# Performance work log

Measured on AMD Instinct MI355X. Metric: run time of the kernel, lower is better.

Reference implementation:

```python
import jax, jax.numpy as jnp
import numpy as np
from jax import lax

DIM = 512
HEADS = 64
EPS_NORM = 1e-12
EPS_BN = 1e-5


def conv1x1(x, w, b):
    # x: [B,Cin,H,W], w: [Cout,Cin,1,1]
    y = lax.conv_general_dilated(x, w, (1, 1), 'SAME',
                                 dimension_numbers=('NCHW', 'OIHW', 'NCHW'))
    return y + b[None, :, None, None]


def dwconv3x3(x, w, b):
    # depthwise: w: [C,1,3,3], groups=C
    c = x.shape[1]
    y = lax.conv_general_dilated(x, w, (1, 1), 'SAME',
                                 dimension_numbers=('NCHW', 'OIHW', 'NCHW'),
                                 feature_group_count=c)
    return y + b[None, :, None, None]


def l2norm(x):
    # normalize along last axis, torch F.normalize semantics
    n = jnp.sqrt(jnp.sum(x * x, axis=-1, keepdims=True))
    return x / jnp.maximum(n, EPS_NORM)


def setup_inputs() -> dict:
    key = jax.random.key(0)
    ks = jax.random.split(key, 12)
    b, c, h, w = 2, DIM, 128, 128
    s = lambda *sh: 0.02
    inp = {
        'hsi': jax.random.normal(ks[0], (b, c, h, w), jnp.float32),
        'lidar': jax.random.normal(ks[1], (b, c, h, w), jnp.float32),
        'hsi_qkv_w': jax.random.normal(ks[2], (3 * c, c, 1, 1), jnp.float32) * 0.02,
        'hsi_qkv_b': jnp.zeros((3 * c,), jnp.float32),
        'lidar_qkv_w': jax.random.normal(ks[3], (3 * c, c, 1, 1), jnp.float32) * 0.02,
        'lidar_qkv_b': jnp.zeros((3 * c,), jnp.float32),
        'hsi_dw_w': jax.random.normal(ks[4], (3 * c, 1, 3, 3), jnp.float32) * 0.1,
        'hsi_dw_b': jnp.zeros((3 * c,), jnp.float32),
        'lidar_dw_w': jax.random.normal(ks[5], (3 * c, 1, 3, 3), jnp.float32) * 0.1,
        'lidar_dw_b': jnp.zeros((3 * c,), jnp.float32),
        'temp1': jnp.ones((HEADS, 1, 1), jnp.float32),
        'temp2': jnp.ones((HEADS, 1, 1), jnp.float32),
        'proj_w': jax.random.normal(ks[6], (c // 8, c // 4, 1, 1), jnp.float32) * 0.1,
        'proj_b': jnp.zeros((c // 8,), jnp.float32),
        'bn_gamma': jnp.ones((c // 8,), jnp.float32),
        'bn_beta': jnp.zeros((c // 8,), jnp.float32),
        'bn_mean': jnp.zeros((c // 8,), jnp.float32),
        'bn_var': jnp.ones((c // 8,), jnp.float32),
    }
    return inp


def reference(hsi, lidar, hsi_qkv_w, hsi_qkv_b, lidar_qkv_w, lidar_qkv_b,
              hsi_dw_w, hsi_dw_b, lidar_dw_w, lidar_dw_b, temp1, temp2,
              proj_w, proj_b, bn_gamma, bn_beta, bn_mean, bn_var):
    b, c, h, w = hsi.shape
    head = HEADS
    ch = c // head  # per-head channel (=8)
    hw = h * w

    def qkv(x, qkv_w, qkv_b, dw_w, dw_b):
        y = conv1x1(x, qkv_w, qkv_b)
        y = dwconv3x3(y, dw_w, dw_b)
        q, k, v = jnp.split(y, 3, axis=1)
        # b (head ch) h w -> b head ch (h w)
        r = lambda t: t.reshape(b, head, ch, hw)
        return r(q), r(k), r(v)

    hq, hk, hv = qkv(hsi, hsi_qkv_w, hsi_qkv_b, hsi_dw_w, hsi_dw_b)
    lq, lk, lv = qkv(lidar, lidar_qkv_w, lidar_qkv_b, lidar_dw_w, lidar_dw_b)

    q1, k2 = l2norm(hq), l2norm(lk)
    q2, k1 = l2norm(lq), l2norm(hk)

    # channel-attention scores: [b, head, ch, ch]
    attn1 = jnp.einsum('bhcn,bhdn->bhcd', q1, k2) * temp1[None]
    attn2 = jnp.einsum('bhcn,bhdn->bhcd', q2, k1) * temp2[None]

    # conv-based score fusion: cat -> 1x1 conv -> BN (eval) -> ReLU
    attn_cat = jnp.concatenate([attn1, attn2], axis=1)  # [b, 2*head, ch, ch]
    fused = conv1x1(attn_cat, proj_w, proj_b)           # [b, head, ch, ch]
    fused = (fused - bn_mean[None, :, None, None]) / jnp.sqrt(bn_var + EPS_BN)[None, :, None, None]
    fused = fused * bn_gamma[None, :, None, None] + bn_beta[None, :, None, None]
    fused = jax.nn.relu(fused)

    a1 = jax.nn.softmax(fused + attn1, axis=-1)
    a2 = jax.nn.softmax(fused + attn2, axis=-1)
    # dropout is identity in eval mode

    hsi_out = jnp.einsum('bhcd,bhdn->bhcn', a1, hv) + hv
    lidar_out = jnp.einsum('bhcd,bhdn->bhcn', a2, lv) + lv

    hsi_out = hsi_out.reshape(b, c, h, w) + hsi
    lidar_out = lidar_out.reshape(b, c, h, w) + lidar
    return hsi_out, lidar_out
```

## Files before the change

kernel.cpp:

```cpp
#include <hip/hip_runtime.h>
#include <hip/hip_bf16.h>

#define B2    2
#define C     512
#define HH    128
#define WW    128
#define HW    16384
#define HEADS 64

typedef __attribute__((ext_vector_type(8))) short bf16x8;
typedef __attribute__((ext_vector_type(4))) float f32x4;
typedef __attribute__((ext_vector_type(4))) unsigned u32x4;

__device__ __forceinline__ float b2f(short s) {
    union { unsigned u; float f; } x;
    x.u = ((unsigned)(unsigned short)s) << 16;
    return x.f;
}
__device__ __forceinline__ short f2b(float f) {
    unsigned u; __builtin_memcpy(&u, &f, 4);
    unsigned r = u + 0x7FFFu + ((u >> 16) & 1u);
    return (short)(r >> 16);
}
__device__ __forceinline__ unsigned cvt_pk(float lo, float hi) {
    unsigned r;
    asm("v_cvt_pk_bf16_f32 %0, %1, %2" : "=v"(r) : "v"(lo), "v"(hi));
    return r;
}

__device__ __forceinline__ void conv8(
    const short* __restrict__ plane, int row, int lane, int cg,
    const float* __restrict__ w9, float bias0, float* o)
{
    #pragma unroll
    for (int i = 0; i < 8; ++i) o[i] = bias0;
    #pragma unroll
    for (int dr = 0; dr < 3; ++dr) {
        const int r2 = row + dr - 1;
        const bool ok = (unsigned)r2 < (unsigned)HH;
        bf16x8 v = {0, 0, 0, 0, 0, 0, 0, 0};
        if (ok) v = *(const bf16x8*)(plane + (size_t)r2 * WW);
        float rv[10];
        #pragma unroll
        for (int j = 0; j < 8; ++j) rv[1 + j] = b2f(v[j]);
        const float lf = __shfl(rv[8], lane - 1);
        const float rt = __shfl(rv[1], lane + 1);
        rv[0] = (cg == 0)  ? 0.f : lf;
        rv[9] = (cg == 15) ? 0.f : rt;
        const float w0 = w9[dr * 3], w1 = w9[dr * 3 + 1], w2 = w9[dr * 3 + 2];
        #pragma unroll
        for (int i = 0; i < 8; ++i)
            o[i] += w0 * rv[i] + w1 * rv[i + 1] + w2 * rv[i + 2];
    }
}

#define BM 128
#define BN 128
#define BK 32
#define LDK 40

struct GemmJob  { const float* X; const float* W; const float* bias; short* Y; int co_off; };
struct GemmJobs { GemmJob j[8]; };

__global__ __launch_bounds__(256) void k_gemm(GemmJobs jobs)
{
    __shared__ __align__(16) short As[BM * LDK];
    __shared__ __align__(16) short Bs[BN * LDK];

    unsigned bx = blockIdx.x, by = blockIdx.y, bz = blockIdx.z;
    {
        const unsigned nx = gridDim.x, ny = gridDim.y, nz = gridDim.z;
        const unsigned nwg = nx * ny * nz;
        if ((nwg & 7u) == 0u) {
            const unsigned hw = bx + nx * (by + ny * bz);
            const unsigned lid = (hw & 7u) * (nwg >> 3) + (hw >> 3);
            bx = lid % nx;
            const unsigned rest = lid / nx;
            by = rest % ny;
            bz = rest / ny;
        }
    }

    const GemmJob jb = jobs.j[bz];
    const float* X    = jb.X;
    const float* Wm   = jb.W;
    const float* bias = jb.bias;
    short*       Y    = jb.Y;
    const int co_off  = jb.co_off;

    const int co0 = bx * BM;
    const int p0  = by * BN;

    const int t = threadIdx.x;
    const int lane = t & 63, wv = t >> 6;
    const int wm = (wv & 1) << 6, wn = (wv >> 1) << 6;
    const int l15 = lane & 15, quad = lane >> 4;
    const int rm = t & 127;
    const int kc = (t >> 7) << 4;

    f32x4 acc[4][4] = {};

    for (int kk = 0; kk < C; kk += BK) {
        const float* asrc = Wm + (size_t)(co_off + co0 + rm) * C + kk + kc;
        unsigned au[4];
        #pragma unroll
        for (int j = 0; j < 2; ++j) {
            f32x4 v = *(const f32x4*)(asrc + j * 4);
            au[2 * j]     = cvt_pk(v[0], v[1]);
            au[2 * j + 1] = cvt_pk(v[2], v[3]);
        }
        unsigned au2[4];
        #pragma unroll
        for (int j = 0; j < 2; ++j) {
            f32x4 v = *(const f32x4*)(asrc + 8 + j * 4);
            au2[2 * j]     = cvt_pk(v[0], v[1]);
            au2[2 * j + 1] = cvt_pk(v[2], v[3]);
        }
        const float* bsrc = X + (size_t)(kk + kc) * HW + p0 + rm;
        float bv[16];
        #pragma unroll
        for (int j = 0; j < 16; ++j) bv[j] = bsrc[(size_t)j * HW];
        unsigned bu[8];
        #pragma unroll
        for (int j = 0; j < 8; ++j) bu[j] = cvt_pk(bv[2 * j], bv[2 * j + 1]);

        *(u32x4*)&As[rm * LDK + kc]     = *(const u32x4*)au;
        *(u32x4*)&As[rm * LDK + kc + 8] = *(const u32x4*)au2;
        *(u32x4*)&Bs[rm * LDK + kc]     = *(const u32x4*)bu;
        *(u32x4*)&Bs[rm * LDK + kc + 8] = *(const u32x4*)(bu + 4);
        __syncthreads();

        bf16x8 af[4], bfr[4];
        #pragma unroll
        for (int i = 0; i < 4; ++i)
            af[i]  = *(const bf16x8*)&As[(wm + i * 16 + l15) * LDK + quad * 8];
        #pragma unroll
        for (int i = 0; i < 4; ++i)
            bfr[i] = *(const bf16x8*)&Bs[(wn + i * 16 + l15) * LDK + quad * 8];
        #pragma unroll
        for (int i = 0; i < 4; ++i)
            #pragma unroll
            for (int j = 0; j < 4; ++j)
                acc[i][j] = __builtin_amdgcn_mfma_f32_16x16x32_bf16(af[i], bfr[j], acc[i][j], 0, 0, 0);
        __syncthreads();
    }

    #pragma unroll
    for (int i = 0; i < 4; ++i) {
        #pragma unroll
        for (int r = 0; r < 4; ++r) {
            const int co = co0 + wm + i * 16 + quad * 4 + r;
            const float bv = bias[co_off + co];
            #pragma unroll
            for (int j = 0; j < 4; ++j) {
                const int p = p0 + wn + j * 16 + l15;
                Y[(size_t)co * HW + p] = f2b(acc[i][j][r] + bv);
            }
        }
    }
}

struct StatsJobs { const short* q[4]; const short* k[4]; };

__global__ __launch_bounds__(256) void k_stats(
    StatsJobs sj,
    const float* __restrict__ dwh_w, const float* __restrict__ dwh_b,
    const float* __restrict__ dwl_w, const float* __restrict__ dwl_b,
    float* __restrict__ dot1, float* __restrict__ dot2, float* __restrict__ sumsq,
    int job0)
{
    const int chunk = blockIdx.x;
    const int h = blockIdx.y;
    const int z = blockIdx.z;
    const int job = job0 + z;
    const int b = job >> 1, type = job & 1;

    const int t = threadIdx.x;
    const int lane = t & 63, w = t >> 6;
    const int ch = lane & 15, g = lane >> 4;
    const bool isq = (ch < 8);

    const float* dw = isq ? (type ? dwl_w : dwh_w) : (type ? dwh_w : dwl_w);
    const float* db = isq ? (type ? dwl_b : dwh_b) : (type ? dwh_b : dwl_b);
    const int crow = isq ? (h * 8 + ch) : (C + h * 8 + ch - 8);
    float w9[9];
    #pragma unroll
    for (int i = 0; i < 9; ++i) w9[i] = dw[crow * 9 + i];
    const float bias0 = db[crow];

    const short* plane = isq ? (sj.q[z] + (size_t)(h * 8 + ch) * HW)
                             : (sj.k[z] + (size_t)(h * 8 + (ch - 8)) * HW);

    f32x4 acc = {0.f, 0.f, 0.f, 0.f};
    float s2 = 0.f;

    for (int cr = 0; cr < 4; ++cr) {
        const int row = chunk * 16 + w * 4 + cr;
        #pragma unroll
        for (int cc = 0; cc < 4; ++cc) {
            const int px0 = cc * 32 + g * 8;
            float o[8];
            #pragma unroll
            for (int i = 0; i < 8; ++i) o[i] = bias0;
            #pragma unroll
            for (int dr = 0; dr < 3; ++dr) {
                const int r2 = row + dr - 1;
                const bool ok = (unsigned)r2 < (unsigned)HH;
                const short* rp = plane + (size_t)r2 * WW;
                bf16x8 v = {0, 0, 0, 0, 0, 0, 0, 0};
                short sl = 0, sr = 0;
                if (ok) {
                    v = *(const bf16x8*)(rp + px0);
                    if (px0 > 0)      sl = rp[px0 - 1];
                    if (px0 + 8 < WW) sr = rp[px0 + 8];
                }
                float rv[10];
                rv[0] = b2f(sl); rv[9] = b2f(sr);
                #pragma unroll
                for (int j = 0; j < 8; ++j) rv[1 + j] = b2f(v[j]);
                const float w0 = w9[dr * 3], w1 = w9[dr * 3 + 1], w2 = w9[dr * 3 + 2];
                #pragma unroll
                for (int i = 0; i < 8; ++i)
                    o[i] += w0 * rv[i] + w1 * rv[i + 1] + w2 * rv[i + 2];
            }
            #pragma unroll
            for (int i = 0; i < 8; ++i) s2 += o[i] * o[i];
            unsigned pu[4];
            #pragma unroll
            for (int p = 0; p < 4; ++p) pu[p] = cvt_pk(o[2 * p], o[2 * p + 1]);
            bf16x8 f; __builtin_memcpy(&f, pu, 16);
            acc = __builtin_amdgcn_mfma_f32_16x16x32_bf16(f, f, acc, 0, 0, 0);
        }
    }

    float* dotp = (type ? dot2 : dot1) + ((size_t)(b * HEADS + h) << 6);
    #pragma unroll
    for (int r = 0; r < 4; ++r) {
        const int rowc = g * 4 + r;
        if (rowc < 8 && ch >= 8)
            atomicAdd(&dotp[rowc * 8 + (ch - 8)], acc[r]);
    }
    s2 += __shfl_down(s2, 32);
    s2 += __shfl_down(s2, 16);
    if (g == 0) {
        float* sp = isq
            ? &sumsq[((type * 2) * 2 + b) * C + h * 8 + ch]
            : &sumsq[((type * 2 + 1) * 2 + b) * C + h * 8 + (ch - 8)];
        atomicAdd(sp, s2);
    }
}

__global__ __launch_bounds__(256) void k_fuse(
    const float* __restrict__ dot1, const float* __restrict__ dot2,
    const float* __restrict__ sumsq,
    const float* __restrict__ temp1, const float* __restrict__ temp2,
    const float* __restrict__ pw, const float* __restrict__ pb,
    const float* __restrict__ g, const float* __restrict__ be,
    const float* __restrict__ mu, const float* __restrict__ var,
    float* __restrict__ a1, float* __restrict__ a2)
{
    __shared__ float cat[128 * 64];
    __shared__ float fus[64 * 64];
    const int b = blockIdx.x;
    const int t = threadIdx.x;
    const float EPS = 1e-12f;

    for (int idx = t; idx < 128 * 64; idx += 256) {
        const int ic = idx >> 6, ij = idx & 63, i = ij >> 3, j = ij & 7;
        const int is2 = ic >> 6, h = ic & 63;
        const float* dp = is2 ? dot2 : dot1;
        const int qkk = is2 * 2, kkk = is2 * 2 + 1;
        const float nq = sqrtf(sumsq[(qkk * 2 + b) * C + h * 8 + i]);
        const float nk = sqrtf(sumsq[(kkk * 2 + b) * C + h * 8 + j]);
        const float tv = is2 ? temp2[h] : temp1[h];
        const float d = dp[((size_t)(b * HEADS + h) << 6) + ij];
        cat[idx] = d / (fmaxf(nq, EPS) * fmaxf(nk, EPS)) * tv;
    }
    __syncthreads();

    for (int idx = t; idx < 64 * 64; idx += 256) {
        const int hd = idx >> 6, ij = idx & 63;
        float acc = pb[hd];
        for (int ic = 0; ic < 128; ++ic)
            acc += pw[hd * 128 + ic] * cat[ic * 64 + ij];
        const float sc = g[hd] / sqrtf(var[hd] + 1e-5f);
        const float v = (acc - mu[hd]) * sc + be[hd];
        fus[idx] = fmaxf(v, 0.f);
    }
    __syncthreads();

    for (int r = t; r < 512; r += 256) {
        const int hd = r >> 3, i = r & 7;
        float v[8], mx, sum;
        mx = -1e30f;
        #pragma unroll
        for (int j = 0; j < 8; ++j) { v[j] = fus[(hd << 6) + i * 8 + j] + cat[(hd << 6) + i * 8 + j]; mx = fmaxf(mx, v[j]); }
        sum = 0.f;
        #pragma unroll
        for (int j = 0; j < 8; ++j) { v[j] = __expf(v[j] - mx); sum += v[j]; }
        #pragma unroll
        for (int j = 0; j < 8; ++j) a1[((size_t)(b * HEADS + hd) << 6) + i * 8 + j] = v[j] / sum;
        mx = -1e30f;
        #pragma unroll
        for (int j = 0; j < 8; ++j) { v[j] = fus[(hd << 6) + i * 8 + j] + cat[((64 + hd) << 6) + i * 8 + j]; mx = fmaxf(mx, v[j]); }
        sum = 0.f;
        #pragma unroll
        for (int j = 0; j < 8; ++j) { v[j] = __expf(v[j] - mx); sum += v[j]; }
        #pragma unroll
        for (int j = 0; j < 8; ++j) a2[((size_t)(b * HEADS + hd) << 6) + i * 8 + j] = v[j] / sum;
    }
}

__global__ __launch_bounds__(256) void k_out(
    const short* __restrict__ vslab, long long vstride, int vrowoff,
    const float* __restrict__ hsi, const float* __restrict__ lidar,
    const float* __restrict__ dwh_w, const float* __restrict__ dwh_b,
    const float* __restrict__ dwl_w, const float* __restrict__ dwl_b,
    const float* __restrict__ a1, const float* __restrict__ a2,
    float* __restrict__ out)
{
    __shared__ float A[64];
    __shared__ float wv[72], bvs[8];
    const int chunk = blockIdx.x, h = blockIdx.y, zb = blockIdx.z;
    const int s = zb >> 1, b = zb & 1;
    const int t = threadIdx.x;

    const float* x   = (s ? lidar : hsi) + (size_t)b * C * HW;
    const float* dww = s ? dwl_w : dwh_w;
    const float* dwb = s ? dwl_b : dwh_b;
    const float* Ag  = (s ? a2 : a1) + ((size_t)(b * HEADS + h) << 6);
    if (t < 64) A[t] = Ag[t] + (((t >> 3) == (t & 7)) ? 1.0f : 0.0f);
    if (t < 72) wv[t] = dww[(2 * C + h * 8) * 9 + t];
    if (t < 8)  bvs[t] = dwb[2 * C + h * 8 + t];
    __syncthreads();

    const int lane = t & 63, cg = t & 15;
    const int row = chunk * 16 + (t >> 4);
    const int col0 = cg << 3;

    const short* ybase = vslab + (size_t)zb * (size_t)vstride
                       + (size_t)(vrowoff + h * 8) * HW + col0;
    const float* xbase = x + (size_t)(h * 8) * HW + (size_t)row * WW + col0;
    float* obase = out + ((size_t)((s * B2 + b) * C + h * 8)) * HW + (size_t)row * WW + col0;

    float o[8][8];
    #pragma unroll
    for (int i = 0; i < 8; ++i)
        #pragma unroll
        for (int px = 0; px < 8; ++px) o[i][px] = 0.f;

    #pragma unroll
    for (int d = 0; d < 8; ++d) {
        float vd[8];
        conv8(ybase + (size_t)d * HW, row, lane, cg, wv + d * 9, bvs[d], vd);
        #pragma unroll
        for (int i = 0; i < 8; ++i) {
            const float ad = A[i * 8 + d];
            #pragma unroll
            for (int px = 0; px < 8; ++px) o[i][px] += ad * vd[px];
        }
    }

    #pragma unroll
    for (int i = 0; i < 8; ++i) {
        f32x4 x0 = *(const f32x4*)(xbase + (size_t)i * HW);
        f32x4 x1 = *(const f32x4*)(xbase + (size_t)i * HW + 4);
        f32x4 o0 = { o[i][0] + x0[0], o[i][1] + x0[1], o[i][2] + x0[2], o[i][3] + x0[3] };
        f32x4 o1 = { o[i][4] + x1[0], o[i][5] + x1[1], o[i][6] + x1[2], o[i][7] + x1[3] };
        *(f32x4*)(obase + (size_t)i * HW)     = o0;
        *(f32x4*)(obase + (size_t)i * HW + 4) = o1;
    }
}

extern "C" void kernel_launch(void* const* d_in, const int* in_sizes, int n_in,
                              void* d_out, int out_size, void* d_ws, size_t ws_size,
                              hipStream_t stream)
{
    const float* hsi  = (const float*)d_in[0];
    const float* lidar= (const float*)d_in[1];
    const float* hqw  = (const float*)d_in[2];
    const float* hqb  = (const float*)d_in[3];
    const float* lqw  = (const float*)d_in[4];
    const float* lqb  = (const float*)d_in[5];
    const float* hdw  = (const float*)d_in[6];
    const float* hdb  = (const float*)d_in[7];
    const float* ldw  = (const float*)d_in[8];
    const float* ldb  = (const float*)d_in[9];
    const float* t1   = (const float*)d_in[10];
    const float* t2   = (const float*)d_in[11];
    const float* pw   = (const float*)d_in[12];
    const float* pb   = (const float*)d_in[13];
    const float* bg   = (const float*)d_in[14];
    const float* bb   = (const float*)d_in[15];
    const float* bm   = (const float*)d_in[16];
    const float* bvv  = (const float*)d_in[17];

    char* ws = (char*)d_ws;
    float* dot1  = (float*)ws;
    float* dot2  = dot1 + 2 * HEADS * 64;
    float* sumsq = dot2 + 2 * HEADS * 64;
    float* a1    = sumsq + 4 * 2 * C;
    float* a2    = a1 + 2 * HEADS * 64;
    short* slab  = (short*)(ws + 147456);

    const size_t statbytes = (size_t)(2 * HEADS * 64 * 2 + 4 * 2 * C) * sizeof(float);
    hipMemsetAsync(dot1, 0, statbytes, stream);

    const size_t planeBytes  = (size_t)C * HW * sizeof(short);
    const size_t imgBytes    = 3 * planeBytes;
    const size_t needMerged  = 147456 + 4 * imgBytes;
    const size_t needR3      = 147456 + 8 * planeBytes;

    const size_t imgS = (size_t)3 * C * HW;

    if (ws_size >= needMerged) {
        GemmJobs jj;
        const float* imgs[4] = { hsi, hsi + (size_t)C * HW, lidar, lidar + (size_t)C * HW };
        const float* wms[4]  = { hqw, hqw, lqw, lqw };
        const float* bs[4]   = { hqb, hqb, lqb, lqb };
        for (int img = 0; img < 4; ++img)
            jj.j[img] = { imgs[img], wms[img], bs[img], slab + (size_t)img * imgS, 0 };
        for (int i = 4; i < 8; ++i) jj.j[i] = jj.j[0];
        k_gemm<<<dim3(12, 128, 4), 256, 0, stream>>>(jj);

        StatsJobs sj;
        for (int job = 0; job < 4; ++job) {
            const int b = job >> 1, type = job & 1;
            sj.q[job] = slab + (size_t)(type * 2 + b) * imgS;
            sj.k[job] = slab + (size_t)((1 - type) * 2 + b) * imgS + (size_t)C * HW;
        }
        k_stats<<<dim3(8, 64, 4), 256, 0, stream>>>(
            sj, hdw, hdb, ldw, ldb, dot1, dot2, sumsq, 0);

        k_fuse<<<dim3(2, 1, 1), 256, 0, stream>>>(dot1, dot2, sumsq, t1, t2,
                                                  pw, pb, bg, bb, bm, bvv, a1, a2);
        k_out<<<dim3(8, 64, 4), 256, 0, stream>>>(
            slab, (long long)imgS, 2 * C, hsi, lidar,
            hdw, hdb, ldw, ldb, a1, a2, (float*)d_out);
    } else if (ws_size >= needR3) {
        GemmJobs jj;
        for (int job = 0; job < 4; ++job) {
            const int b = job >> 1, type = job & 1;
            const float* qx = (type ? lidar : hsi) + (size_t)b * C * HW;
            const float* kx = (type ? hsi : lidar) + (size_t)b * C * HW;
            const float* qw = type ? lqw : hqw;  const float* qb = type ? lqb : hqb;
            const float* kw = type ? hqw : lqw;  const float* kb = type ? hqb : lqb;
            jj.j[2 * job]     = { qx, qw, qb, slab + (size_t)(2 * job) * C * HW,     0 };
            jj.j[2 * job + 1] = { kx, kw, kb, slab + (size_t)(2 * job + 1) * C * HW, C };
        }
        k_gemm<<<dim3(4, 128, 8), 256, 0, stream>>>(jj);

        StatsJobs sj;
        for (int job = 0; job < 4; ++job) {
            sj.q[job] = slab + (size_t)(2 * job) * C * HW;
            sj.k[job] = slab + (size_t)(2 * job + 1) * C * HW;
        }
        k_stats<<<dim3(8, 64, 4), 256, 0, stream>>>(
            sj, hdw, hdb, ldw, ldb, dot1, dot2, sumsq, 0);

        GemmJobs vj;
        vj.j[0] = { hsi,                    hqw, hqb, slab,                      2 * C };
        vj.j[1] = { hsi   + (size_t)C * HW, hqw, hqb, slab + (size_t)C * HW,     2 * C };
        vj.j[2] = { lidar,                  lqw, lqb, slab + (size_t)2 * C * HW, 2 * C };
        vj.j[3] = { lidar + (size_t)C * HW, lqw, lqb, slab + (size_t)3 * C * HW, 2 * C };
        for (int i = 4; i < 8; ++i) vj.j[i] = vj.j[0];
        k_gemm<<<dim3(4, 128, 4), 256, 0, stream>>>(vj);

        k_fuse<<<dim3(2, 1, 1), 256, 0, stream>>>(dot1, dot2, sumsq, t1, t2,
                                                  pw, pb, bg, bb, bm, bvv, a1, a2);
        k_out<<<dim3(8, 64, 4), 256, 0, stream>>>(
            slab, (long long)((size_t)C * HW), 0, hsi, lidar,
            hdw, hdb, ldw, ldb, a1, a2, (float*)d_out);
    } else {
        for (int b = 0; b < 2; ++b) {
            for (int type = 0; type < 2; ++type) {
                const float* qx = (type ? lidar : hsi) + (size_t)b * C * HW;
                const float* kx = (type ? hsi : lidar) + (size_t)b * C * HW;
                const float* qw = type ? lqw : hqw;  const float* qb = type ? lqb : hqb;
                const float* kw = type ? hqw : lqw;  const float* kb = type ? hqb : lqb;
                GemmJobs jj;
                jj.j[0] = { qx, qw, qb, slab,                  0 };
                jj.j[1] = { kx, kw, kb, slab + (size_t)C * HW, C };
                for (int i = 2; i < 8; ++i) jj.j[i] = jj.j[0];
                k_gemm<<<dim3(4, 128, 2), 256, 0, stream>>>(jj);
                StatsJobs sj;
                sj.q[0] = slab;
                sj.k[0] = slab + (size_t)C * HW;
                for (int i = 1; i < 4; ++i) { sj.q[i] = sj.q[0]; sj.k[i] = sj.k[0]; }
                k_stats<<<dim3(8, 64, 1), 256, 0, stream>>>(
                    sj, hdw, hdb, ldw, ldb, dot1, dot2, sumsq, b * 2 + type);
            }
        }
        GemmJobs vj;
        vj.j[0] = { hsi,                    hqw, hqb, slab,                      2 * C };
        vj.j[1] = { hsi   + (size_t)C * HW, hqw, hqb, slab + (size_t)C * HW,     2 * C };
        vj.j[2] = { lidar,                  lqw, lqb, slab + (size_t)2 * C * HW, 2 * C };
        vj.j[3] = { lidar + (size_t)C * HW, lqw, lqb, slab + (size_t)3 * C * HW, 2 * C };
        for (int i = 4; i < 8; ++i) vj.j[i] = vj.j[0];
        k_gemm<<<dim3(4, 128, 4), 256, 0, stream>>>(vj);

        k_fuse<<<dim3(2, 1, 1), 256, 0, stream>>>(dot1, dot2, sumsq, t1, t2,
                                                  pw, pb, bg, bb, bm, bvv, a1, a2);
        k_out<<<dim3(8, 64, 4), 256, 0, stream>>>(
            slab, (long long)((size_t)C * HW), 0, hsi, lidar,
            hdw, hdb, ldw, ldb, a1, a2, (float*)d_out);
    }
}
```

Measured before the change: 844.0 us.

## Pre-convert QKV weights and inputs to bf16 before GEMM

Adds a conversion kernel that turns fp32 weights and input images into bf16 in workspace. A new GEMM then reads bf16 operands directly, instead of converting fp32 inside the GEMM tile loads. The four image GEMMs are split into two rounds (hsi, then lidar) so that two image-sized bf16 buffers can be reused. This cuts GEMM load bandwidth and removes repeated in-loop conversion, at the cost of extra conversion passes, more kernel launches and a larger workspace requirement.

```diff
diff --git a/kernel.cpp b/kernel.cpp
--- a/kernel.cpp
+++ b/kernel.cpp
@@ -54,10 +54,140 @@
     }
 }
 
+struct CvtJobs { const float* src[4]; short* dst[4]; int n8[4]; };
+
+__global__ __launch_bounds__(256) void k_cvt(CvtJobs cj)
+{
+    const int z = blockIdx.z;
+    const float* __restrict__ src = cj.src[z];
+    unsigned* __restrict__ dst = (unsigned*)cj.dst[z];
+    const int n8 = cj.n8[z];
+    for (int i = blockIdx.x * 256 + threadIdx.x; i < n8; i += gridDim.x * 256) {
+        f32x4 v0 = *(const f32x4*)(src + (size_t)i * 8);
+        f32x4 v1 = *(const f32x4*)(src + (size_t)i * 8 + 4);
+        u32x4 o = { cvt_pk(v0[0], v0[1]), cvt_pk(v0[2], v0[3]),
+                    cvt_pk(v1[0], v1[1]), cvt_pk(v1[2], v1[3]) };
+        *(u32x4*)(dst + (size_t)i * 4) = o;
+    }
+}
+
 #define BM 128
 #define BN 128
 #define BK 32
 #define LDK 40
+
+struct G2Job  { const short* Xb; const short* Wb; const float* bias; short* Y; };
+struct G2Jobs { G2Job j[2]; };
+
+__global__ __launch_bounds__(256) void k_gemm2(G2Jobs jobs)
+{
+    __shared__ __align__(16) short As[BM * LDK];
+    __shared__ __align__(16) short Bs[BN * LDK];
+
+    unsigned bx = blockIdx.x, by = blockIdx.y, bz = blockIdx.z;
+    {
+        const unsigned nx = gridDim.x, ny = gridDim.y, nz = gridDim.z;
+        const unsigned nwg = nx * ny * nz;
+        if ((nwg & 7u) == 0u) {
+            const unsigned hw = bx + nx * (by + ny * bz);
+            const unsigned lid = (hw & 7u) * (nwg >> 3) + (hw >> 3);
+            bx = lid % nx;
+            const unsigned rest = lid / nx;
+            by = rest % ny;
+            bz = rest / ny;
+        }
+    }
+
+    const G2Job jb = jobs.j[bz];
+    const short* __restrict__ Xb = jb.Xb;
+    const short* __restrict__ Wb = jb.Wb;
+    const float* __restrict__ bias = jb.bias;
+    short* __restrict__ Y = jb.Y;
+
+    const int co0 = bx * BM;
+    const int p0  = by * BN;
+
+    const int t = threadIdx.x;
+    const int lane = t & 63, wv = t >> 6;
+    const int wm = (wv & 1) << 6, wn = (wv >> 1) << 6;
+    const int l15 = lane & 15, quad = lane >> 4;
+    const int rm  = t & 127;
+    const int kcA = (t >> 7) << 4;
+    const int pp  = t & 63;
+    const int ksB = (t >> 6) << 3;
+
+    const short* aptr = Wb + (size_t)(co0 + rm) * C + kcA;
+    const unsigned* xptr = (const unsigned*)Xb + (size_t)ksB * (HW / 2)
+                         + (p0 >> 1) + pp;
+
+    bf16x8 a0 = *(const bf16x8*)aptr;
+    bf16x8 a1 = *(const bf16x8*)(aptr + 8);
+    unsigned bd[8];
+    #pragma unroll
+    for (int i = 0; i < 8; ++i) bd[i] = xptr[(size_t)i * (HW / 2)];
+
+    f32x4 acc[4][4] = {};
+
+    for (int kk = 0; kk < C; kk += BK) {
+        *(bf16x8*)&As[rm * LDK + kcA]     = a0;
+        *(bf16x8*)&As[rm * LDK + kcA + 8] = a1;
+        unsigned lo[4], hi[4];
+        #pragma unroll
+        for (int j = 0; j < 4; ++j) {
+            lo[j] = (bd[2 * j] & 0xFFFFu) | (bd[2 * j + 1] << 16);
+            hi[j] = (bd[2 * j] >> 16) | (bd[2 * j + 1] & 0xFFFF0000u);
+        }
+        {
+            const int r0 = 2 * pp, r1 = 2 * pp + 1;
+            const unsigned off0 = (unsigned)((r0 * LDK + ksB) * 2) ^ ((((unsigned)r0 >> 3) & 7u) << 4);
+            const unsigned off1 = (unsigned)((r1 * LDK + ksB) * 2) ^ ((((unsigned)r1 >> 3) & 7u) << 4);
+            u32x4 wlo = { lo[0], lo[1], lo[2], lo[3] };
+            u32x4 whi = { hi[0], hi[1], hi[2], hi[3] };
+            *(u32x4*)((char*)Bs + off0) = wlo;
+            *(u32x4*)((char*)Bs + off1) = whi;
+        }
+        __syncthreads();
+
+        if (kk + BK < C) {
+            a0 = *(const bf16x8*)(aptr + kk + BK);
+            a1 = *(const bf16x8*)(aptr + kk + BK + 8);
+            #pragma unroll
+            for (int i = 0; i < 8; ++i)
+                bd[i] = xptr[(size_t)(kk + BK + i) * (HW / 2)];
+        }
+
+        bf16x8 af[4], bfr[4];
+        #pragma unroll
+        for (int i = 0; i < 4; ++i)
+            af[i] = *(const bf16x8*)&As[(wm + i * 16 + l15) * LDK + quad * 8];
+        #pragma unroll
+        for (int i = 0; i < 4; ++i) {
+            const int rr = wn + i * 16 + l15;
+            const unsigned offr = (unsigned)((rr * LDK + quad * 8) * 2) ^ ((((unsigned)rr >> 3) & 7u) << 4);
+            bfr[i] = *(const bf16x8*)((char*)Bs + offr);
+        }
+        #pragma unroll
+        for (int i = 0; i < 4; ++i)
+            #pragma unroll
+            for (int j = 0; j < 4; ++j)
+                acc[i][j] = __builtin_amdgcn_mfma_f32_16x16x32_bf16(af[i], bfr[j], acc[i][j], 0, 0, 0);
+        __syncthreads();
+    }
+
+    #pragma unroll
+    for (int i = 0; i < 4; ++i) {
+        #pragma unroll
+        for (int r = 0; r < 4; ++r) {
+            const int co = co0 + wm + i * 16 + quad * 4 + r;
+            const float bv = bias[co];
+            #pragma unroll
+            for (int j = 0; j < 4; ++j) {
+                const int p = p0 + wn + j * 16 + l15;
+                Y[(size_t)co * HW + p] = f2b(acc[i][j][r] + bv);
+            }
+        }
+    }
+}
 
 struct GemmJob  { const float* X; const float* W; const float* bias; short* Y; int co_off; };
 struct GemmJobs { GemmJob j[8]; };
@@ -408,12 +538,59 @@
 
     const size_t planeBytes  = (size_t)C * HW * sizeof(short);
     const size_t imgBytes    = 3 * planeBytes;
+    const size_t imgS        = (size_t)3 * C * HW;
+    const size_t wbS         = (size_t)3 * C * C;
+    const size_t xbS         = (size_t)C * HW;
+
+    const size_t needFull    = 147456 + (4 * imgS + 2 * wbS + 2 * xbS) * sizeof(short);
     const size_t needMerged  = 147456 + 4 * imgBytes;
     const size_t needR3      = 147456 + 8 * planeBytes;
 
-    const size_t imgS = (size_t)3 * C * HW;
-
-    if (ws_size >= needMerged) {
+    if (ws_size >= needFull) {
+        short* Wbh = slab + 4 * imgS;
+        short* Wbl = Wbh + wbS;
+        short* Xb0 = Wbl + wbS;
+        short* Xb1 = Xb0 + xbS;
+
+        CvtJobs c1;
+        c1.src[0] = hqw;                     c1.dst[0] = Wbh; c1.n8[0] = (int)(wbS / 8);
+        c1.src[1] = lqw;                     c1.dst[1] = Wbl; c1.n8[1] = (int)(wbS / 8);
+        c1.src[2] = hsi;                     c1.dst[2] = Xb0; c1.n8[2] = (int)(xbS / 8);
+        c1.src[3] = hsi + (size_t)C * HW;    c1.dst[3] = Xb1; c1.n8[3] = (int)(xbS / 8);
+        k_cvt<<<dim3(1024, 1, 4), 256, 0, stream>>>(c1);
+
+        G2Jobs g1;
+        g1.j[0] = { Xb0, Wbh, hqb, slab + 0 * imgS };
+        g1.j[1] = { Xb1, Wbh, hqb, slab + 1 * imgS };
+        k_gemm2<<<dim3(12, 128, 2), 256, 0, stream>>>(g1);
+
+        CvtJobs c2;
+        c2.src[0] = lidar;                   c2.dst[0] = Xb0; c2.n8[0] = (int)(xbS / 8);
+        c2.src[1] = lidar + (size_t)C * HW;  c2.dst[1] = Xb1; c2.n8[1] = (int)(xbS / 8);
+        c2.src[2] = hqw;                     c2.dst[2] = Wbh; c2.n8[2] = 0;
+        c2.src[3] = hqw;                     c2.dst[3] = Wbh; c2.n8[3] = 0;
+        k_cvt<<<dim3(1024, 1, 2), 256, 0, stream>>>(c2);
+
+        G2Jobs g2;
+        g2.j[0] = { Xb0, Wbl, lqb, slab + 2 * imgS };
+        g2.j[1] = { Xb1, Wbl, lqb, slab + 3 * imgS };
+        k_gemm2<<<dim3(12, 128, 2), 256, 0, stream>>>(g2);
+
+        StatsJobs sj;
+        for (int job = 0; job < 4; ++job) {
+            const int b = job >> 1, type = job & 1;
+            sj.q[job] = slab + (size_t)(type * 2 + b) * imgS;
+            sj.k[job] = slab + (size_t)((1 - type) * 2 + b) * imgS + (size_t)C * HW;
+        }
+        k_stats<<<dim3(8, 64, 4), 256, 0, stream>>>(
+            sj, hdw, hdb, ldw, ldb, dot1, dot2, sumsq, 0);
+
+        k_fuse<<<dim3(2, 1, 1), 256, 0, stream>>>(dot1, dot2, sumsq, t1, t2,
+                                                  pw, pb, bg, bb, bm, bvv, a1, a2);
+        k_out<<<dim3(8, 64, 4), 256, 0, stream>>>(
+            slab, (long long)imgS, 2 * C, hsi, lidar,
+            hdw, hdb, ldw, ldb, a1, a2, (float*)d_out);
+    } else if (ws_size >= needMerged) {
         GemmJobs jj;
         const float* imgs[4] = { hsi, hsi + (size_t)C * HW, lidar, lidar + (size_t)C * HW };
         const float* wms[4]  = { hqw, hqw, lqw, lqw };
```

New measurement: 763.4 us. 9.5% less time.
